# Optimization experiments

Hardware: AMD Instinct MI355X
Metric: run time of the kernel (lower is better)

Reference implementation:

```python
import jax, jax.numpy as jnp
import numpy as np

B, N, E, M, F_, H, K, D, T = 16, 100, 9900, 50, 64, 128, 20, 2, 8
EPS = 1e-5

def _lin(key, fin, fout):
    k1, _ = jax.random.split(key)
    w = jax.random.normal(k1, (fin, fout), jnp.float32) * np.float32(np.sqrt(2.0 / (fin + fout)))
    b = jnp.full((fout,), 0.1, jnp.float32)
    return w, b

def setup_inputs():
    key = jax.random.key(0)
    ks = jax.random.split(key, 16)
    pairs = np.array([(i, j) for i in range(N) for j in range(N) if i != j], np.int64)
    rel_rec = np.zeros((E, N), np.float32); rel_rec[np.arange(E), pairs[:, 0]] = 1.0
    rel_send = np.zeros((E, N), np.float32); rel_send[np.arange(E), pairs[:, 1]] = 1.0
    W1g, b1g = _lin(ks[0], 2 * F_, H)
    W2g, b2g = _lin(ks[1], H, H)
    W1h, b1h = _lin(ks[2], F_, H)
    W2h, b2h = _lin(ks[3], H, H)
    Wo1, bo1 = _lin(ks[4], 2 * H, H)
    Wa, ba = _lin(ks[5], H, K)
    Wm, bm = _lin(ks[6], H, K * D)
    ones = jnp.ones((H,), jnp.float32); zeros = jnp.zeros((H,), jnp.float32)
    return {
        'data': jax.random.normal(ks[7], (B, N, T, D), jnp.float32),
        'rel_rec_g': jnp.asarray(rel_rec), 'rel_send_g': jnp.asarray(rel_send),
        'rel_type_g': jax.random.uniform(ks[8], (B, E, 4), jnp.float32),
        'rel_type_hg': jax.random.uniform(ks[9], (B, M, 4), jnp.float32),
        'I_HG': jax.random.uniform(ks[10], (B, N, M), jnp.float32),
        'v_combined': jax.random.normal(ks[11], (B, N, F_), jnp.float32),
        'W1g': W1g, 'b1g': b1g, 'g1g': ones, 'be1g': zeros,
        'W2g': W2g, 'b2g': b2g, 'g2g': ones, 'be2g': zeros,
        'W1h': W1h, 'b1h': b1h, 'g1h': ones, 'be1h': zeros,
        'W2h': W2h, 'b2h': b2h, 'g2h': ones, 'be2h': zeros,
        'Wo1': Wo1, 'bo1': bo1, 'Wa': Wa, 'ba': ba, 'Wm': Wm, 'bm': bm,
        'output_steps': 8,
    }

def _lrelu(x):
    return jnp.where(x >= 0, x, 0.01 * x)

def _bn(x, g, b):
    # training-mode BatchNorm1d: batch statistics over the flattened row dim
    mu = x.mean(0); var = x.var(0)
    return (x - mu) / jnp.sqrt(var + EPS) * g + b

def reference(data, rel_rec_g, rel_send_g, rel_type_g, rel_type_hg, I_HG, v_combined,
              W1g, b1g, g1g, be1g, W2g, b2g, g2g, be2g,
              W1h, b1h, g1h, be1h, W2h, b2h, g2h, be2h,
              Wo1, bo1, Wa, ba, Wm, bm, output_steps):
    inputs = jnp.swapaxes(data, 1, 2)                                # [B,T,N,D]
    # ---- CG edge branch (step-invariant: depends only on v_combined) ----
    recv = jnp.einsum('en,bnf->bef', rel_rec_g, v_combined)
    send = jnp.einsum('en,bnf->bef', rel_send_g, v_combined)
    pre = jnp.concatenate([recv, send], -1)                          # [B,E,2F]
    x = pre.reshape(B * E, 2 * F_)
    msg = _lrelu(_bn(x @ W1g + b1g, g1g, be1g))
    msg = _lrelu(_bn(msg @ W2g + b2g, g2g, be2g)).reshape(B, E, H)
    # (msg[...,None] * Z).mean(-1) == msg * Z.mean(-1) since Z is independent of the hid dim
    all_g = _lrelu(msg * rel_type_g.mean(-1, keepdims=True) + pre)   # identity shortcut (n_in_mlp == n_hid)
    hidden_g = jnp.einsum('beh,en->bnh', all_g, rel_send_g) / D
    # ---- hypergraph branch ----
    pre_h = jnp.einsum('bnm,bnf->bmf', I_HG, v_combined)             # [B,M,F]
    xh = pre_h.reshape(B * M, F_)
    mh = _lrelu(_bn(xh @ W1h + b1h, g1h, be1h))
    mh = _lrelu(_bn(mh @ W2h + b2h, g2h, be2h)).reshape(B, M, H)
    hidden_hg = jnp.einsum('bmh,bnm->bnh', mh * rel_type_hg.mean(-1, keepdims=True), I_HG) / D
    # ---- output heads ----
    v = _lrelu(jnp.concatenate([hidden_g, hidden_hg], -1) @ Wo1 + bo1)  # [B,N,H]
    alpha = jax.nn.softmax(v @ Wa + ba, -1)                          # [B,N,K]
    mu_base = (v @ Wm + bm).reshape(B, N, K, D)
    core = jnp.einsum('bnk,bnkd->bnd', alpha, mu_base)               # sample_core == mixture mean
    nkey = jax.random.key(1234)
    preds, mus = [], []
    ins = inputs[:, 0]                                               # burn_in_steps = 1
    for s in range(output_steps):
        if s > 0:
            ins = preds[-1]
        noise = jax.random.normal(jax.random.fold_in(nkey, s), (B, N, D), jnp.float32)  # sigma == 1
        preds.append(ins + core + noise)
        mus.append(mu_base + ins[:, :, None, :])                     # in-place mu += inputs in torch
    S = output_steps
    preds_out = jnp.swapaxes(jnp.stack(preds, 1), 1, 2)              # [B,N,S,D]
    alphas = jnp.broadcast_to(alpha[:, :, None, :], (B, N, S, K))
    mus_out = jnp.stack(mus, 2)                                      # [B,N,S,K,D]
    sigmas = jnp.ones((B, N, S, K, D), jnp.float32)
    return (preds_out, alphas, mus_out, sigmas)
```

## Files before the change

kernel.cpp:

```cpp
#include <hip/hip_runtime.h>

#define BB 16
#define NN 100
#define EE 9900
#define MM 50
#define FF 64
#define KK 20
#define DD 2
#define ROWS (BB*EE)
#define HROWS (BB*MM)
#define BN_CNT (BB*NN)
#define NTILE (ROWS/64)
#define GEMMB 512
#define EPSF 1e-5f
#define XPITCH 136

typedef __attribute__((ext_vector_type(8))) short bf16x8;
typedef __attribute__((ext_vector_type(4))) float f32x4;

__device__ __forceinline__ float lrelu(float x) { return (x >= 0.f) ? x : 0.01f * x; }

__device__ __forceinline__ unsigned short f2bf(float x) {
  unsigned u = __float_as_uint(x);
  return (unsigned short)((u + 0x7fffu + ((u >> 16) & 1u)) >> 16);
}
__device__ __forceinline__ unsigned pk2(float a, float b) {
  return (unsigned)f2bf(a) | ((unsigned)f2bf(b) << 16);
}
__device__ __forceinline__ float bf2f(unsigned short u) {
  return __uint_as_float(((unsigned)u) << 16);
}

__device__ __forceinline__ void tf2x32(unsigned k0, unsigned k1,
                                       unsigned x0, unsigned x1,
                                       unsigned& o0, unsigned& o1) {
  unsigned ks2 = k0 ^ k1 ^ 0x1BD11BDAu;
  x0 += k0; x1 += k1;
#define TFR(r) { x0 += x1; x1 = (x1 << r) | (x1 >> (32 - r)); x1 ^= x0; }
  TFR(13) TFR(15) TFR(26) TFR(6)   x0 += k1;  x1 += ks2 + 1u;
  TFR(17) TFR(29) TFR(16) TFR(24)  x0 += ks2; x1 += k0 + 2u;
  TFR(13) TFR(15) TFR(26) TFR(6)   x0 += k0;  x1 += k1 + 3u;
  TFR(17) TFR(29) TFR(16) TFR(24)  x0 += k1;  x1 += ks2 + 4u;
  TFR(13) TFR(15) TFR(26) TFR(6)   x0 += ks2; x1 += k0 + 5u;
#undef TFR
  o0 = x0; o1 = x1;
}

__device__ __forceinline__ float bits_to_normal(unsigned bits) {
  float f = __uint_as_float((bits >> 9) | 0x3f800000u) - 1.0f;
  const float lo = -0.99999994f;
  float x = fmaxf(lo, fmaf(f, 2.0f, lo));
  float w = -log1pf(-x * x);
  float p;
  if (w < 5.0f) {
    w = w - 2.5f;
    p = 2.81022636e-08f;
    p = fmaf(p, w, 3.43273939e-07f);
    p = fmaf(p, w, -3.5233877e-06f);
    p = fmaf(p, w, -4.39150654e-06f);
    p = fmaf(p, w, 0.00021858087f);
    p = fmaf(p, w, -0.00125372503f);
    p = fmaf(p, w, -0.00417768164f);
    p = fmaf(p, w, 0.246640727f);
    p = fmaf(p, w, 1.50140941f);
  } else {
    w = sqrtf(w) - 3.0f;
    p = -0.000200214257f;
    p = fmaf(p, w, 0.000100950558f);
    p = fmaf(p, w, 0.00134934322f);
    p = fmaf(p, w, -0.00367342844f);
    p = fmaf(p, w, 0.00573950773f);
    p = fmaf(p, w, -0.0076224613f);
    p = fmaf(p, w, 0.00943887047f);
    p = fmaf(p, w, 1.00167406f);
    p = fmaf(p, w, 2.83297682f);
  }
  return 1.41421356237f * (p * x);
}

struct SmemGemm {
  unsigned short Xt[64 * XPITCH];
  float aColP[132], bColP[132];
  float bsum[128], bssq[128];
};
struct SmemVe {
  float cat[2][256], vres[2][128], lgs[2][KK], mrow[2][KK * DD], alsh[2][KK];
};
struct SmemH {
  float prerow[2][FF];
  float trow[2][128];
};
struct SmemOut {
  float nz[4][8][2], ins[4][8][2], alsh[4][KK];
};

struct Params {
  const float *data, *rtg, *rth, *I_HG, *v;
  const float *W1g, *b1g, *g1g, *be1g, *W2g, *b2g, *g2g, *be2g;
  const float *W1h, *b1h, *g1h, *be1h, *W2h, *b2h, *g2h, *be2h;
  const float *Wo1, *bo1, *Wa, *ba, *Wm, *bm;
  unsigned short *Ybf, *WtG;
  float *stats1, *stats2, *statsh1, *statsh2, *scaleg, *scaleh;
  float *hg, *hh, *y1h, *y2h, *va, *vmu, *vcore, *partials, *partial2;
  float *out;
};


__device__ __forceinline__ void prep_phase(const Params& p, int bid, int nblk, int tid) {
  for (int i = bid * 256 + tid; i < ROWS + HROWS; i += nblk * 256) {
    if (i < ROWS) {
      float4 r = ((const float4*)p.rtg)[i];
      p.scaleg[i] = (r.x + r.y + r.z + r.w) * 0.25f;
    } else {
      float4 r = ((const float4*)p.rth)[i - ROWS];
      p.scaleh[i - ROWS] = (r.x + r.y + r.z + r.w) * 0.25f;
    }
  }
  for (int i = bid * 256 + tid; i < 32768; i += nblk * 256) {
    int w = i >> 14, rem = i & 16383;
    int c = rem & 127, k = rem >> 7;
    const float* W = w ? p.W2g : p.W1g;
    p.WtG[w * 16384 + c * 128 + k] = f2bf(W[k * 128 + c]);
  }
}

template <int MODE>
__device__ __forceinline__ void edge_gemm_phase(
    const Params& p, SmemGemm& sg, int bid, int nblk, int tid,
    const unsigned short* WtG, const unsigned short* Yin, unsigned short* Yout,
    const float* bias, const float* gmm, const float* beta,
    const float* stats_in) {
  const int lane = tid & 63, wid = tid >> 6;
  const int l15 = lane & 15, lq = lane >> 4;
  const int cb = wid * 32;
  const int rsi = tid >> 2, q = tid & 3, k0 = q * 32;

  if (tid < 128) {
    sg.bsum[tid] = 0.f; sg.bssq[tid] = 0.f;
    if (MODE == 1) {
      float s = stats_in[tid], ss = stats_in[128 + tid];
      float mu = s * (1.f / ROWS);
      float var = fmaxf(ss * (1.f / ROWS) - mu * mu, 0.f);
      float rs = 1.f / sqrtf(var + EPSF);
      float a = rs * gmm[tid];
      int pi = tid + (tid >> 5);
      sg.aColP[pi] = a; sg.bColP[pi] = beta[tid] - mu * a;
    }
  }

  const unsigned short* WA = WtG + (cb + l15) * 128 + lq * 8;
  bf16x8 a0[4], a1[4];
#pragma unroll
  for (int kc = 0; kc < 4; ++kc) {
    a0[kc] = *(const bf16x8*)(WA + kc * 32);
    a1[kc] = *(const bf16x8*)(WA + 16 * 128 + kc * 32);
  }
  float4 bi0 = *(const float4*)&bias[cb + lq * 4];
  float4 bi1 = *(const float4*)&bias[cb + 16 + lq * 4];
  f32x4 bv0 = {bi0.x, bi0.y, bi0.z, bi0.w};
  f32x4 bv1 = {bi1.x, bi1.y, bi1.z, bi1.w};
  f32x4 s0 = {0.f,0.f,0.f,0.f}, ss0 = {0.f,0.f,0.f,0.f};
  f32x4 s1 = {0.f,0.f,0.f,0.f}, ss1 = {0.f,0.f,0.f,0.f};

  float4 ra[4], rb[4];
  uint4  rw[4];

  auto LOAD = [&](int tile) {
    if (MODE == 0) {
      int g = tile * 64 + rsi;
      int b = g / EE; int e = g - b * EE;
      int i = e / 99; int jj = e - i * 99; int j = jj + ((jj >= i) ? 1 : 0);
      int vsrc = (q < 2) ? ((b * NN + i) * FF + q * 32)
                         : ((b * NN + j) * FF + (q - 2) * 32);
#pragma unroll
      for (int i2 = 0; i2 < 4; ++i2) {
        ra[i2] = *(const float4*)&p.v[vsrc + i2 * 8];
        rb[i2] = *(const float4*)&p.v[vsrc + i2 * 8 + 4];
      }
    } else {
      const unsigned short* src = Yin + (size_t)(tile * 64 + rsi) * 128 + k0;
#pragma unroll
      for (int i2 = 0; i2 < 4; ++i2) rw[i2] = *(const uint4*)&src[i2 * 8];
    }
  };
  auto WRITE = [&]() {
    if (MODE == 0) {
#pragma unroll
      for (int i2 = 0; i2 < 4; ++i2) {
        uint4 pk;
        pk.x = pk2(ra[i2].x, ra[i2].y); pk.y = pk2(ra[i2].z, ra[i2].w);
        pk.z = pk2(rb[i2].x, rb[i2].y); pk.w = pk2(rb[i2].z, rb[i2].w);
        *(uint4*)&sg.Xt[rsi * XPITCH + k0 + i2 * 8] = pk;
      }
    } else {
#pragma unroll
      for (int i2 = 0; i2 < 4; ++i2) {
        unsigned rr[4] = {rw[i2].x, rw[i2].y, rw[i2].z, rw[i2].w};
        unsigned ow[4];
#pragma unroll
        for (int u = 0; u < 4; ++u) {
          int k = k0 + i2 * 8 + u * 2;
          int p1 = k + (k >> 5);
          float xl = __uint_as_float(rr[u] << 16);
          float xh = __uint_as_float(rr[u] & 0xffff0000u);
          xl = lrelu(fmaf(xl, sg.aColP[p1], sg.bColP[p1]));
          xh = lrelu(fmaf(xh, sg.aColP[p1 + 1], sg.bColP[p1 + 1]));
          ow[u] = pk2(xl, xh);
        }
        uint4 pk; pk.x = ow[0]; pk.y = ow[1]; pk.z = ow[2]; pk.w = ow[3];
        *(uint4*)&sg.Xt[rsi * XPITCH + k0 + i2 * 8] = pk;
      }
    }
  };

  if (MODE == 1) __syncthreads();

  LOAD(bid);
  for (int t = bid; t < NTILE; t += nblk) {
    if (t != bid) __syncthreads();
    WRITE();
    if (t + nblk < NTILE) LOAD(t + nblk);
    __syncthreads();

    f32x4 acc[2][4];
#pragma unroll
    for (int a = 0; a < 2; ++a)
#pragma unroll
      for (int b2 = 0; b2 < 4; ++b2) acc[a][b2] = (f32x4){0.f, 0.f, 0.f, 0.f};
    const unsigned short* Bb = &sg.Xt[l15 * XPITCH + lq * 8];
#pragma unroll
    for (int kc = 0; kc < 4; ++kc) {
      int ko = kc * 32;
#pragma unroll
      for (int rbi = 0; rbi < 4; ++rbi) {
        bf16x8 bfr = *(const bf16x8*)(Bb + rbi * 16 * XPITCH + ko);
        acc[0][rbi] = __builtin_amdgcn_mfma_f32_16x16x32_bf16(a0[kc], bfr, acc[0][rbi], 0, 0, 0);
        acc[1][rbi] = __builtin_amdgcn_mfma_f32_16x16x32_bf16(a1[kc], bfr, acc[1][rbi], 0, 0, 0);
      }
    }

    int r0 = t * 64;
#pragma unroll
    for (int rbi = 0; rbi < 4; ++rbi) {
      size_t r = (size_t)(r0 + rbi * 16 + l15);
      f32x4 y0 = acc[0][rbi] + bv0;
      f32x4 y1 = acc[1][rbi] + bv1;
      uint2 w0; w0.x = pk2(y0.x, y0.y); w0.y = pk2(y0.z, y0.w);
      uint2 w1; w1.x = pk2(y1.x, y1.y); w1.y = pk2(y1.z, y1.w);
      *(uint2*)&Yout[r * 128 + cb + lq * 4] = w0;
      *(uint2*)&Yout[r * 128 + cb + 16 + lq * 4] = w1;
      s0 += y0; ss0 += y0 * y0;
      s1 += y1; ss1 += y1 * y1;
    }
  }

#pragma unroll
  for (int u = 0; u < 4; ++u) {
    atomicAdd(&sg.bsum[cb + lq * 4 + u], s0[u]);
    atomicAdd(&sg.bssq[cb + lq * 4 + u], ss0[u]);
    atomicAdd(&sg.bsum[cb + 16 + lq * 4 + u], s1[u]);
    atomicAdd(&sg.bssq[cb + 16 + lq * 4 + u], ss1[u]);
  }
  __syncthreads();
  if (tid < 128) {
    p.partials[(size_t)bid * 256 + tid] = sg.bsum[tid];
    p.partials[(size_t)bid * 256 + 128 + tid] = sg.bssq[tid];
  }
}

__device__ __forceinline__ void redA_phase(const float* partials, float* partial2,
                                           int nblk, int bid, int tid) {
  if (bid < 32) {
    float s = 0.f;
    for (int r = bid; r < nblk; r += 32) s += partials[(size_t)r * 256 + tid];
    partial2[bid * 256 + tid] = s;
  }
}
__device__ __forceinline__ void redB_phase(const float* partial2, float* stats,
                                           int bid, int tid) {
  if (bid == 0) {
    float s = 0.f;
#pragma unroll
    for (int r = 0; r < 32; ++r) s += partial2[r * 256 + tid];
    stats[tid] = s;
  }
}

__device__ __forceinline__ void recv_phase(const Params& p, int bid, int nblk, int tid) {
  const int sub = tid >> 7, h = tid & 127;
  float s = p.stats2[h], ss = p.stats2[128 + h];
  float mu = s * (1.f / ROWS);
  float var = fmaxf(ss * (1.f / ROWS) - mu * mu, 0.f);
  float rs = 1.f / sqrtf(var + EPSF);
  float a = rs * p.g2g[h]; float bc = p.be2g[h] - mu * a;
  for (int bn = bid * 2 + sub; bn < BN_CNT; bn += 2 * nblk) {
    int b = bn / NN, n = bn - b * NN;
    float sv = (h >= 64) ? p.v[(b * NN + n) * FF + (h - 64)] : 0.f;
    float acc = 0.f;
#pragma unroll 4
    for (int i = 0; i < NN; ++i) {
      if (i == n) continue;
      int e = i * 99 + ((n < i) ? n : n - 1);
      int row = b * EE + e;
      float y = bf2f(p.Ybf[(size_t)row * 128 + h]);
      float msgv = lrelu(y * a + bc);
      float pre = (h < 64) ? p.v[(b * NN + i) * FF + h] : sv;
      float ag = lrelu(fmaf(msgv, p.scaleg[row], pre));
      acc += ag;
    }
    p.hg[bn * 128 + h] = acc * 0.5f;
  }
}

__device__ __forceinline__ void h1_phase(const Params& p, SmemH& sh, int bid, int nblk, int tid) {
  const int sub = tid >> 7, ht = tid & 127;
  for (int bm = bid * 2 + sub; bm < HROWS; bm += 2 * nblk) {
    int b = bm / MM, m = bm - b * MM;
    if (ht < FF) {
      float s = 0.f;
      for (int n = 0; n < NN; ++n)
        s = fmaf(p.I_HG[(b * NN + n) * MM + m], p.v[(b * NN + n) * FF + ht], s);
      sh.prerow[sub][ht] = s;
    }
    __syncthreads();
    float y = p.b1h[ht];
    for (int f = 0; f < FF; ++f) y = fmaf(sh.prerow[sub][f], p.W1h[f * 128 + ht], y);
    p.y1h[bm * 128 + ht] = y;
    __syncthreads();
  }
}

__device__ __forceinline__ void cs_phase(const float* X, float* stats, int bid, int tid) {
  if (bid < 32) {
    int c = bid * 4 + (tid >> 6), rt = tid & 63;
    float s = 0.f, ss = 0.f;
    for (int r = rt; r < HROWS; r += 64) {
      float x = X[(size_t)r * 128 + c];
      s += x; ss += x * x;
    }
    for (int off = 32; off; off >>= 1) {
      s += __shfl_down(s, off, 64);
      ss += __shfl_down(ss, off, 64);
    }
    if (rt == 0) { stats[c] = s; stats[128 + c] = ss; }
  }
}

__device__ __forceinline__ void h2_phase(const Params& p, SmemH& sh, int bid, int nblk, int tid) {
  const int sub = tid >> 7, ht = tid & 127;
  float s = p.statsh1[ht], ss = p.statsh1[128 + ht];
  float mu = s * (1.f / HROWS);
  float var = fmaxf(ss * (1.f / HROWS) - mu * mu, 0.f);
  float rs = 1.f / sqrtf(var + EPSF);
  float a = rs * p.g1h[ht]; float bc = p.be1h[ht] - mu * a;
  for (int bm = bid * 2 + sub; bm < HROWS; bm += 2 * nblk) {
    sh.trow[sub][ht] = lrelu(p.y1h[bm * 128 + ht] * a + bc);
    __syncthreads();
    float y = p.b2h[ht];
    for (int f = 0; f < 128; ++f) y = fmaf(sh.trow[sub][f], p.W2h[f * 128 + ht], y);
    p.y2h[bm * 128 + ht] = y;
    __syncthreads();
  }
}

__device__ __forceinline__ void h3_phase(const Params& p, int bid, int nblk, int tid) {
  const int sub = tid >> 7, h = tid & 127;
  float s = p.statsh2[h], ss = p.statsh2[128 + h];
  float mu = s * (1.f / HROWS);
  float var = fmaxf(ss * (1.f / HROWS) - mu * mu, 0.f);
  float rs = 1.f / sqrtf(var + EPSF);
  float a = rs * p.g2h[h]; float bc = p.be2h[h] - mu * a;
  for (int bn = bid * 2 + sub; bn < BN_CNT; bn += 2 * nblk) {
    int b = bn / NN, n = bn - b * NN;
    float acc = 0.f;
    for (int m = 0; m < MM; ++m) {
      float x = lrelu(p.y2h[(b * MM + m) * 128 + h] * a + bc);
      acc = fmaf(x * p.scaleh[b * MM + m], p.I_HG[(b * NN + n) * MM + m], acc);
    }
    p.hh[bn * 128 + h] = acc * 0.5f;
  }
}

__device__ __forceinline__ void ve_phase(const Params& p, SmemVe& sv, int bid, int nblk, int tid) {
  const int sub = tid >> 7, ht = tid & 127;
  for (int bn = bid * 2 + sub; bn < BN_CNT; bn += 2 * nblk) {
    sv.cat[sub][ht] = p.hg[bn * 128 + ht];
    sv.cat[sub][128 + ht] = p.hh[bn * 128 + ht];
    __syncthreads();
    float vv = p.bo1[ht];
    for (int k = 0; k < 256; ++k)
      vv = fmaf(sv.cat[sub][k], p.Wo1[k * 128 + ht], vv);
    sv.vres[sub][ht] = lrelu(vv);
    __syncthreads();
    if (ht < KK) {
      float s = p.ba[ht];
      for (int f = 0; f < 128; ++f) s = fmaf(sv.vres[sub][f], p.Wa[f * KK + ht], s);
      sv.lgs[sub][ht] = s;
    } else if (ht >= 64 && ht < 64 + KK * DD) {
      int c = ht - 64;
      float s = p.bm[c];
      for (int f = 0; f < 128; ++f) s = fmaf(sv.vres[sub][f], p.Wm[f * (KK * DD) + c], s);
      sv.mrow[sub][c] = s;
      p.vmu[bn * (KK * DD) + c] = s;
    }
    __syncthreads();
    if (ht < KK) {
      float mx = sv.lgs[sub][0];
      for (int k2 = 1; k2 < KK; ++k2) mx = fmaxf(mx, sv.lgs[sub][k2]);
      float se = 0.f;
      for (int k2 = 0; k2 < KK; ++k2) se += expf(sv.lgs[sub][k2] - mx);
      float al = expf(sv.lgs[sub][ht] - mx) / se;
      sv.alsh[sub][ht] = al;
      p.va[bn * KK + ht] = al;
    }
    __syncthreads();
    if (ht < DD) {
      float s = 0.f;
      for (int k2 = 0; k2 < KK; ++k2)
        s = fmaf(sv.alsh[sub][k2], sv.mrow[sub][k2 * DD + ht], s);
      p.vcore[bn * DD + ht] = s;
    }
    __syncthreads();
  }
}

__device__ __forceinline__ void out_phase(const Params& p, SmemOut& so, int bid, int nblk, int tid) {
  const int ut = tid >> 6, t = tid & 63;
  for (int bn = bid * 4 + ut; bn < BN_CNT; bn += 4 * nblk) {
    if (t < 16) {
      int s = t >> 1, d = t & 1;
      unsigned fk0, fk1;
      tf2x32(0u, 1234u, 0u, (unsigned)s, fk0, fk1);
      unsigned flat = (unsigned)(bn * 2 + d);
      unsigned o0, o1;
      tf2x32(fk0, fk1, 0u, flat, o0, o1);
      so.nz[ut][s][d] = bits_to_normal(o0 ^ o1);
    }
    if (t < KK) so.alsh[ut][t] = p.va[bn * KK + t];
    __syncthreads();
    if (t < 2) {
      int d = t;
      float ins0 = p.data[bn * 16 + d];
      float core = p.vcore[bn * 2 + d];
      float pp = ins0;
      for (int s = 0; s < 8; ++s) {
        so.ins[ut][s][d] = pp;
        pp = (pp + core) + so.nz[ut][s][d];
        p.out[(bn * 8 + s) * 2 + d] = pp;
      }
    }
    __syncthreads();
    for (int q = t; q < 160; q += 64) {
      int k = q % KK;
      p.out[25600 + bn * 160 + q] = so.alsh[ut][k];
    }
    for (int q = t; q < 320; q += 64) {
      int s = q / 40, kd = q - s * 40, d = kd & 1;
      p.out[281600 + bn * 320 + q] = p.vmu[bn * 40 + kd] + so.ins[ut][s][d];
    }
    for (int q = t; q < 320; q += 64) p.out[793600 + bn * 320 + q] = 1.0f;
    __syncthreads();
  }
}

__global__ __launch_bounds__(256) void k_prepW(Params p) {
  prep_phase(p, blockIdx.x, gridDim.x, threadIdx.x);
}
__global__ __launch_bounds__(256, 2) void k_gemm0W(Params p) {
  __shared__ __align__(16) SmemGemm sg;
  edge_gemm_phase<0>(p, sg, blockIdx.x, gridDim.x, threadIdx.x, p.WtG, nullptr,
                     p.Ybf, p.b1g, nullptr, nullptr, nullptr);
}
__global__ __launch_bounds__(256, 2) void k_gemm1W(Params p) {
  __shared__ __align__(16) SmemGemm sg;
  edge_gemm_phase<1>(p, sg, blockIdx.x, gridDim.x, threadIdx.x, p.WtG + 16384,
                     p.Ybf, p.Ybf, p.b2g, p.g1g, p.be1g, p.stats1);
}
__global__ __launch_bounds__(256) void k_redAW(const float* partials, float* partial2, int nblk) {
  redA_phase(partials, partial2, nblk, blockIdx.x, threadIdx.x);
}
__global__ __launch_bounds__(256) void k_redBW(const float* partial2, float* stats) {
  redB_phase(partial2, stats, blockIdx.x, threadIdx.x);
}
__global__ __launch_bounds__(256) void k_recvW(Params p) {
  recv_phase(p, blockIdx.x, gridDim.x, threadIdx.x);
}
__global__ __launch_bounds__(256) void k_h1W(Params p) {
  __shared__ SmemH sh;
  h1_phase(p, sh, blockIdx.x, gridDim.x, threadIdx.x);
}
__global__ __launch_bounds__(256) void k_csW(const float* X, float* stats) {
  cs_phase(X, stats, blockIdx.x, threadIdx.x);
}
__global__ __launch_bounds__(256) void k_h2W(Params p) {
  __shared__ SmemH sh;
  h2_phase(p, sh, blockIdx.x, gridDim.x, threadIdx.x);
}
__global__ __launch_bounds__(256) void k_h3W(Params p) {
  h3_phase(p, blockIdx.x, gridDim.x, threadIdx.x);
}
__global__ __launch_bounds__(256) void k_veW(Params p) {
  __shared__ SmemVe sv;
  ve_phase(p, sv, blockIdx.x, gridDim.x, threadIdx.x);
}
__global__ __launch_bounds__(256) void k_outW(Params p) {
  __shared__ SmemOut so;
  out_phase(p, so, blockIdx.x, gridDim.x, threadIdx.x);
}

extern "C" void kernel_launch(void* const* d_in, const int* in_sizes, int n_in,
                              void* d_out, int out_size, void* d_ws, size_t ws_size,
                              hipStream_t stream) {
  char* wsb = (char*)d_ws;

  Params p;
  p.data = (const float*)d_in[0];
  p.rtg  = (const float*)d_in[3];
  p.rth  = (const float*)d_in[4];
  p.I_HG = (const float*)d_in[5];
  p.v    = (const float*)d_in[6];
  p.W1g  = (const float*)d_in[7];
  p.b1g  = (const float*)d_in[8];
  p.g1g  = (const float*)d_in[9];
  p.be1g = (const float*)d_in[10];
  p.W2g  = (const float*)d_in[11];
  p.b2g  = (const float*)d_in[12];
  p.g2g  = (const float*)d_in[13];
  p.be2g = (const float*)d_in[14];
  p.W1h  = (const float*)d_in[15];
  p.b1h  = (const float*)d_in[16];
  p.g1h  = (const float*)d_in[17];
  p.be1h = (const float*)d_in[18];
  p.W2h  = (const float*)d_in[19];
  p.b2h  = (const float*)d_in[20];
  p.g2h  = (const float*)d_in[21];
  p.be2h = (const float*)d_in[22];
  p.Wo1  = (const float*)d_in[23];
  p.bo1  = (const float*)d_in[24];
  p.Wa   = (const float*)d_in[25];
  p.ba   = (const float*)d_in[26];
  p.Wm   = (const float*)d_in[27];
  p.bm   = (const float*)d_in[28];

  p.Ybf     = (unsigned short*)wsb;
  p.stats1  = (float*)(wsb + 40550400);
  p.stats2  = p.stats1 + 256;
  p.statsh1 = p.stats2 + 256;
  p.statsh2 = p.statsh1 + 256;
  p.scaleg  = (float*)(wsb + 40550400 + 4096);
  p.scaleh  = p.scaleg + ROWS;
  p.hg      = p.scaleh + HROWS;
  p.hh      = p.hg + BN_CNT * 128;
  p.y1h     = p.hh + BN_CNT * 128;
  p.y2h     = p.y1h + HROWS * 128;
  p.va      = p.y2h + HROWS * 128;
  p.vmu     = p.va + BN_CNT * KK;
  p.vcore   = p.vmu + BN_CNT * KK * DD;
  p.WtG     = (unsigned short*)(p.vcore + BN_CNT * DD);
  p.partials = (float*)(p.WtG + 2 * 16384);
  p.partial2 = p.partials + (size_t)GEMMB * 256;
  p.out     = (float*)d_out;

  k_prepW<<<256, 256, 0, stream>>>(p);
  k_gemm0W<<<GEMMB, 256, 0, stream>>>(p);
  k_redAW<<<32, 256, 0, stream>>>(p.partials, p.partial2, GEMMB);
  k_redBW<<<1, 256, 0, stream>>>(p.partial2, p.stats1);
  k_gemm1W<<<GEMMB, 256, 0, stream>>>(p);
  k_redAW<<<32, 256, 0, stream>>>(p.partials, p.partial2, GEMMB);
  k_redBW<<<1, 256, 0, stream>>>(p.partial2, p.stats2);
  k_recvW<<<800, 256, 0, stream>>>(p);
  k_h1W<<<400, 256, 0, stream>>>(p);
  k_csW<<<32, 256, 0, stream>>>(p.y1h, p.statsh1);
  k_h2W<<<400, 256, 0, stream>>>(p);
  k_csW<<<32, 256, 0, stream>>>(p.y2h, p.statsh2);
  k_h3W<<<800, 256, 0, stream>>>(p);
  k_veW<<<800, 256, 0, stream>>>(p);
  k_outW<<<400, 256, 0, stream>>>(p);
}
```

Measured before the change: 303.3 us.

## Fuse reductions into last-block epilogues and merge tail phases into one kernel

Batch-statistic reductions now run in the last block to finish each GEMM or hypergraph kernel, using an atomic counter, which removes the separate redA/redB/cs launches. The receive, hypergraph-aggregate, output-head and output-write phases are merged into a single per-node kernel, so the hg/hh/va/vmu/vcore intermediates no longer go through global memory. GEMM grid grows to 825 blocks with launch bounds raised to 4 waves per SIMD. This cuts the launch count from 15 to 6. In exchange, the final reduction is serialized in one block, and the counters depend on being reset in the prep kernel each call.

Result: slower. 624.7 us (+106.0%).

```diff
diff --git a/kernel.cpp b/kernel.cpp
--- a/kernel.cpp
+++ b/kernel.cpp
@@ -11,7 +11,7 @@
 #define HROWS (BB*MM)
 #define BN_CNT (BB*NN)
 #define NTILE (ROWS/64)
-#define GEMMB 512
+#define GEMMB 825
 #define EPSF 1e-5f
 #define XPITCH 136
 
@@ -83,16 +83,6 @@
   float aColP[132], bColP[132];
   float bsum[128], bssq[128];
 };
-struct SmemVe {
-  float cat[2][256], vres[2][128], lgs[2][KK], mrow[2][KK * DD], alsh[2][KK];
-};
-struct SmemH {
-  float prerow[2][FF];
-  float trow[2][128];
-};
-struct SmemOut {
-  float nz[4][8][2], ins[4][8][2], alsh[4][KK];
-};
 
 struct Params {
   const float *data, *rtg, *rth, *I_HG, *v;
@@ -101,13 +91,15 @@
   const float *Wo1, *bo1, *Wa, *ba, *Wm, *bm;
   unsigned short *Ybf, *WtG;
   float *stats1, *stats2, *statsh1, *statsh2, *scaleg, *scaleh;
-  float *hg, *hh, *y1h, *y2h, *va, *vmu, *vcore, *partials, *partial2;
+  float *y1h, *y2h, *partials;
+  unsigned *cnt;
   float *out;
 };
 
-
-__device__ __forceinline__ void prep_phase(const Params& p, int bid, int nblk, int tid) {
-  for (int i = bid * 256 + tid; i < ROWS + HROWS; i += nblk * 256) {
+__global__ __launch_bounds__(256) void k_prepW(Params p) {
+  const int bid = blockIdx.x, tid = threadIdx.x;
+  if (bid == 0 && tid < 4) p.cnt[tid] = 0;
+  for (int i = bid * 256 + tid; i < ROWS + HROWS; i += 256 * 256) {
     if (i < ROWS) {
       float4 r = ((const float4*)p.rtg)[i];
       p.scaleg[i] = (r.x + r.y + r.z + r.w) * 0.25f;
@@ -116,11 +108,14 @@
       p.scaleh[i - ROWS] = (r.x + r.y + r.z + r.w) * 0.25f;
     }
   }
-  for (int i = bid * 256 + tid; i < 32768; i += nblk * 256) {
-    int w = i >> 14, rem = i & 16383;
-    int c = rem & 127, k = rem >> 7;
-    const float* W = w ? p.W2g : p.W1g;
-    p.WtG[w * 16384 + c * 128 + k] = f2bf(W[k * 128 + c]);
+  {
+    int i = bid * 256 + tid;
+    if (i < 32768) {
+      int w = i >> 14, rem = i & 16383;
+      int c = rem & 127, k = rem >> 7;
+      const float* W = w ? p.W2g : p.W1g;
+      p.WtG[w * 16384 + c * 128 + k] = f2bf(W[k * 128 + c]);
+    }
   }
 }
 
@@ -268,244 +263,203 @@
   }
 }
 
-__device__ __forceinline__ void redA_phase(const float* partials, float* partial2,
-                                           int nblk, int bid, int tid) {
-  if (bid < 32) {
+__device__ __forceinline__ void lastblock_stats(const Params& p, float* stats,
+                                                unsigned* cnt, int nblk, int tid) {
+  __shared__ int isLast;
+  __threadfence();
+  __syncthreads();
+  if (tid == 0) isLast = (atomicAdd(cnt, 1u) == (unsigned)(nblk - 1));
+  __syncthreads();
+  if (isLast) {
+    __threadfence();
     float s = 0.f;
-    for (int r = bid; r < nblk; r += 32) s += partials[(size_t)r * 256 + tid];
-    partial2[bid * 256 + tid] = s;
-  }
-}
-__device__ __forceinline__ void redB_phase(const float* partial2, float* stats,
-                                           int bid, int tid) {
-  if (bid == 0) {
+#pragma unroll 5
+    for (int r = 0; r < nblk; ++r) s += p.partials[(size_t)r * 256 + tid];
+    stats[tid] = s;
+  }
+}
+
+__global__ __launch_bounds__(256, 4) void k_gemm0W(Params p) {
+  __shared__ __align__(16) SmemGemm sg;
+  edge_gemm_phase<0>(p, sg, blockIdx.x, GEMMB, threadIdx.x, p.WtG, nullptr,
+                     p.Ybf, p.b1g, nullptr, nullptr, nullptr);
+  lastblock_stats(p, p.stats1, p.cnt + 0, GEMMB, threadIdx.x);
+}
+__global__ __launch_bounds__(256, 4) void k_gemm1W(Params p) {
+  __shared__ __align__(16) SmemGemm sg;
+  edge_gemm_phase<1>(p, sg, blockIdx.x, GEMMB, threadIdx.x, p.WtG + 16384,
+                     p.Ybf, p.Ybf, p.b2g, p.g1g, p.be1g, p.stats1);
+  lastblock_stats(p, p.stats2, p.cnt + 1, GEMMB, threadIdx.x);
+}
+
+__device__ __forceinline__ void lastblock_colstats(const float* X, float* stats,
+                                                   unsigned* cnt, int nblk, int tid) {
+  __shared__ int isLast;
+  __shared__ float rs[128], rss[128];
+  __threadfence();
+  __syncthreads();
+  if (tid == 0) isLast = (atomicAdd(cnt, 1u) == (unsigned)(nblk - 1));
+  __syncthreads();
+  if (isLast) {
+    __threadfence();
+    int c = tid & 127, half = tid >> 7;
+    float s = 0.f, ss = 0.f;
+    for (int r = half * 400; r < half * 400 + 400; ++r) {
+      float x = X[(size_t)r * 128 + c];
+      s += x; ss += x * x;
+    }
+    if (half) { rs[c] = s; rss[c] = ss; }
+    __syncthreads();
+    if (!half) { stats[c] = s + rs[c]; stats[128 + c] = ss + rss[c]; }
+  }
+}
+
+__global__ __launch_bounds__(256) void k_h1W(Params p) {
+  __shared__ float prerow[2][FF];
+  const int bid = blockIdx.x, tid = threadIdx.x;
+  const int sub = tid >> 7, ht = tid & 127;
+  const int bm = bid * 2 + sub;
+  const int b = bm / MM, m = bm - b * MM;
+  if (ht < FF) {
     float s = 0.f;
-#pragma unroll
-    for (int r = 0; r < 32; ++r) s += partial2[r * 256 + tid];
-    stats[tid] = s;
-  }
-}
-
-__device__ __forceinline__ void recv_phase(const Params& p, int bid, int nblk, int tid) {
-  const int sub = tid >> 7, h = tid & 127;
-  float s = p.stats2[h], ss = p.stats2[128 + h];
-  float mu = s * (1.f / ROWS);
-  float var = fmaxf(ss * (1.f / ROWS) - mu * mu, 0.f);
+    for (int n = 0; n < NN; ++n)
+      s = fmaf(p.I_HG[(b * NN + n) * MM + m], p.v[(b * NN + n) * FF + ht], s);
+    prerow[sub][ht] = s;
+  }
+  __syncthreads();
+  float y = p.b1h[ht];
+  for (int f = 0; f < FF; ++f) y = fmaf(prerow[sub][f], p.W1h[f * 128 + ht], y);
+  p.y1h[bm * 128 + ht] = y;
+  lastblock_colstats(p.y1h, p.statsh1, p.cnt + 2, 400, tid);
+}
+
+__global__ __launch_bounds__(256) void k_h2W(Params p) {
+  __shared__ float trow[2][128];
+  const int bid = blockIdx.x, tid = threadIdx.x;
+  const int sub = tid >> 7, ht = tid & 127;
+  const int bm = bid * 2 + sub;
+  float s = p.statsh1[ht], ss = p.statsh1[128 + ht];
+  float mu = s * (1.f / HROWS);
+  float var = fmaxf(ss * (1.f / HROWS) - mu * mu, 0.f);
   float rs = 1.f / sqrtf(var + EPSF);
-  float a = rs * p.g2g[h]; float bc = p.be2g[h] - mu * a;
-  for (int bn = bid * 2 + sub; bn < BN_CNT; bn += 2 * nblk) {
-    int b = bn / NN, n = bn - b * NN;
-    float sv = (h >= 64) ? p.v[(b * NN + n) * FF + (h - 64)] : 0.f;
+  float a = rs * p.g1h[ht]; float bc = p.be1h[ht] - mu * a;
+  trow[sub][ht] = lrelu(p.y1h[bm * 128 + ht] * a + bc);
+  __syncthreads();
+  float y = p.b2h[ht];
+  for (int f = 0; f < 128; ++f) y = fmaf(trow[sub][f], p.W2h[f * 128 + ht], y);
+  p.y2h[bm * 128 + ht] = y;
+  lastblock_colstats(p.y2h, p.statsh2, p.cnt + 3, 400, tid);
+}
+
+struct SmemFin {
+  float cat[2][256];
+  float vres[2][128];
+  float lgs[2][KK], mrow[2][KK * DD], alsh[2][KK], vcore[2][DD];
+  float nz[2][8][2], ins[2][8][2];
+};
+
+__global__ __launch_bounds__(256) void k_finW(Params p) {
+  __shared__ __align__(16) SmemFin sm;
+  const int tid = threadIdx.x;
+  const int sub = tid >> 7, ht = tid & 127;
+  const int bn = blockIdx.x * 2 + sub;
+  const int b = bn / NN, n = bn - b * NN;
+
+  if (ht < 16) {
+    int s = ht >> 1, d = ht & 1;
+    unsigned fk0, fk1;
+    tf2x32(0u, 1234u, 0u, (unsigned)s, fk0, fk1);
+    unsigned flat = (unsigned)(bn * 2 + d);
+    unsigned o0, o1;
+    tf2x32(fk0, fk1, 0u, flat, o0, o1);
+    sm.nz[sub][s][d] = bits_to_normal(o0 ^ o1);
+  }
+
+  {
+    float s = p.stats2[ht], ss = p.stats2[128 + ht];
+    float mu = s * (1.f / ROWS);
+    float var = fmaxf(ss * (1.f / ROWS) - mu * mu, 0.f);
+    float rs = 1.f / sqrtf(var + EPSF);
+    float a = rs * p.g2g[ht]; float bc = p.be2g[ht] - mu * a;
+    float sv = (ht >= 64) ? p.v[(b * NN + n) * FF + (ht - 64)] : 0.f;
     float acc = 0.f;
 #pragma unroll 4
     for (int i = 0; i < NN; ++i) {
       if (i == n) continue;
       int e = i * 99 + ((n < i) ? n : n - 1);
       int row = b * EE + e;
-      float y = bf2f(p.Ybf[(size_t)row * 128 + h]);
+      float y = bf2f(p.Ybf[(size_t)row * 128 + ht]);
       float msgv = lrelu(y * a + bc);
-      float pre = (h < 64) ? p.v[(b * NN + i) * FF + h] : sv;
-      float ag = lrelu(fmaf(msgv, p.scaleg[row], pre));
-      acc += ag;
-    }
-    p.hg[bn * 128 + h] = acc * 0.5f;
-  }
-}
-
-__device__ __forceinline__ void h1_phase(const Params& p, SmemH& sh, int bid, int nblk, int tid) {
-  const int sub = tid >> 7, ht = tid & 127;
-  for (int bm = bid * 2 + sub; bm < HROWS; bm += 2 * nblk) {
-    int b = bm / MM, m = bm - b * MM;
-    if (ht < FF) {
-      float s = 0.f;
-      for (int n = 0; n < NN; ++n)
-        s = fmaf(p.I_HG[(b * NN + n) * MM + m], p.v[(b * NN + n) * FF + ht], s);
-      sh.prerow[sub][ht] = s;
-    }
-    __syncthreads();
-    float y = p.b1h[ht];
-    for (int f = 0; f < FF; ++f) y = fmaf(sh.prerow[sub][f], p.W1h[f * 128 + ht], y);
-    p.y1h[bm * 128 + ht] = y;
-    __syncthreads();
-  }
-}
-
-__device__ __forceinline__ void cs_phase(const float* X, float* stats, int bid, int tid) {
-  if (bid < 32) {
-    int c = bid * 4 + (tid >> 6), rt = tid & 63;
-    float s = 0.f, ss = 0.f;
-    for (int r = rt; r < HROWS; r += 64) {
-      float x = X[(size_t)r * 128 + c];
-      s += x; ss += x * x;
-    }
-    for (int off = 32; off; off >>= 1) {
-      s += __shfl_down(s, off, 64);
-      ss += __shfl_down(ss, off, 64);
-    }
-    if (rt == 0) { stats[c] = s; stats[128 + c] = ss; }
-  }
-}
-
-__device__ __forceinline__ void h2_phase(const Params& p, SmemH& sh, int bid, int nblk, int tid) {
-  const int sub = tid >> 7, ht = tid & 127;
-  float s = p.statsh1[ht], ss = p.statsh1[128 + ht];
-  float mu = s * (1.f / HROWS);
-  float var = fmaxf(ss * (1.f / HROWS) - mu * mu, 0.f);
-  float rs = 1.f / sqrtf(var + EPSF);
-  float a = rs * p.g1h[ht]; float bc = p.be1h[ht] - mu * a;
-  for (int bm = bid * 2 + sub; bm < HROWS; bm += 2 * nblk) {
-    sh.trow[sub][ht] = lrelu(p.y1h[bm * 128 + ht] * a + bc);
-    __syncthreads();
-    float y = p.b2h[ht];
-    for (int f = 0; f < 128; ++f) y = fmaf(sh.trow[sub][f], p.W2h[f * 128 + ht], y);
-    p.y2h[bm * 128 + ht] = y;
-    __syncthreads();
-  }
-}
-
-__device__ __forceinline__ void h3_phase(const Params& p, int bid, int nblk, int tid) {
-  const int sub = tid >> 7, h = tid & 127;
-  float s = p.statsh2[h], ss = p.statsh2[128 + h];
-  float mu = s * (1.f / HROWS);
-  float var = fmaxf(ss * (1.f / HROWS) - mu * mu, 0.f);
-  float rs = 1.f / sqrtf(var + EPSF);
-  float a = rs * p.g2h[h]; float bc = p.be2h[h] - mu * a;
-  for (int bn = bid * 2 + sub; bn < BN_CNT; bn += 2 * nblk) {
-    int b = bn / NN, n = bn - b * NN;
+      float pre = (ht < 64) ? p.v[(b * NN + i) * FF + ht] : sv;
+      acc += lrelu(fmaf(msgv, p.scaleg[row], pre));
+    }
+    sm.cat[sub][ht] = acc * 0.5f;
+  }
+  {
+    float s = p.statsh2[ht], ss = p.statsh2[128 + ht];
+    float mu = s * (1.f / HROWS);
+    float var = fmaxf(ss * (1.f / HROWS) - mu * mu, 0.f);
+    float rs = 1.f / sqrtf(var + EPSF);
+    float a = rs * p.g2h[ht]; float bc = p.be2h[ht] - mu * a;
     float acc = 0.f;
     for (int m = 0; m < MM; ++m) {
-      float x = lrelu(p.y2h[(b * MM + m) * 128 + h] * a + bc);
+      float x = lrelu(p.y2h[(b * MM + m) * 128 + ht] * a + bc);
       acc = fmaf(x * p.scaleh[b * MM + m], p.I_HG[(b * NN + n) * MM + m], acc);
     }
-    p.hh[bn * 128 + h] = acc * 0.5f;
-  }
-}
-
-__device__ __forceinline__ void ve_phase(const Params& p, SmemVe& sv, int bid, int nblk, int tid) {
-  const int sub = tid >> 7, ht = tid & 127;
-  for (int bn = bid * 2 + sub; bn < BN_CNT; bn += 2 * nblk) {
-    sv.cat[sub][ht] = p.hg[bn * 128 + ht];
-    sv.cat[sub][128 + ht] = p.hh[bn * 128 + ht];
-    __syncthreads();
-    float vv = p.bo1[ht];
-    for (int k = 0; k < 256; ++k)
-      vv = fmaf(sv.cat[sub][k], p.Wo1[k * 128 + ht], vv);
-    sv.vres[sub][ht] = lrelu(vv);
-    __syncthreads();
-    if (ht < KK) {
-      float s = p.ba[ht];
-      for (int f = 0; f < 128; ++f) s = fmaf(sv.vres[sub][f], p.Wa[f * KK + ht], s);
-      sv.lgs[sub][ht] = s;
-    } else if (ht >= 64 && ht < 64 + KK * DD) {
-      int c = ht - 64;
-      float s = p.bm[c];
-      for (int f = 0; f < 128; ++f) s = fmaf(sv.vres[sub][f], p.Wm[f * (KK * DD) + c], s);
-      sv.mrow[sub][c] = s;
-      p.vmu[bn * (KK * DD) + c] = s;
-    }
-    __syncthreads();
-    if (ht < KK) {
-      float mx = sv.lgs[sub][0];
-      for (int k2 = 1; k2 < KK; ++k2) mx = fmaxf(mx, sv.lgs[sub][k2]);
-      float se = 0.f;
-      for (int k2 = 0; k2 < KK; ++k2) se += expf(sv.lgs[sub][k2] - mx);
-      float al = expf(sv.lgs[sub][ht] - mx) / se;
-      sv.alsh[sub][ht] = al;
-      p.va[bn * KK + ht] = al;
-    }
-    __syncthreads();
-    if (ht < DD) {
-      float s = 0.f;
-      for (int k2 = 0; k2 < KK; ++k2)
-        s = fmaf(sv.alsh[sub][k2], sv.mrow[sub][k2 * DD + ht], s);
-      p.vcore[bn * DD + ht] = s;
-    }
-    __syncthreads();
-  }
-}
-
-__device__ __forceinline__ void out_phase(const Params& p, SmemOut& so, int bid, int nblk, int tid) {
-  const int ut = tid >> 6, t = tid & 63;
-  for (int bn = bid * 4 + ut; bn < BN_CNT; bn += 4 * nblk) {
-    if (t < 16) {
-      int s = t >> 1, d = t & 1;
-      unsigned fk0, fk1;
-      tf2x32(0u, 1234u, 0u, (unsigned)s, fk0, fk1);
-      unsigned flat = (unsigned)(bn * 2 + d);
-      unsigned o0, o1;
-      tf2x32(fk0, fk1, 0u, flat, o0, o1);
-      so.nz[ut][s][d] = bits_to_normal(o0 ^ o1);
-    }
-    if (t < KK) so.alsh[ut][t] = p.va[bn * KK + t];
-    __syncthreads();
-    if (t < 2) {
-      int d = t;
-      float ins0 = p.data[bn * 16 + d];
-      float core = p.vcore[bn * 2 + d];
-      float pp = ins0;
-      for (int s = 0; s < 8; ++s) {
-        so.ins[ut][s][d] = pp;
-        pp = (pp + core) + so.nz[ut][s][d];
-        p.out[(bn * 8 + s) * 2 + d] = pp;
-      }
-    }
-    __syncthreads();
-    for (int q = t; q < 160; q += 64) {
-      int k = q % KK;
-      p.out[25600 + bn * 160 + q] = so.alsh[ut][k];
-    }
-    for (int q = t; q < 320; q += 64) {
-      int s = q / 40, kd = q - s * 40, d = kd & 1;
-      p.out[281600 + bn * 320 + q] = p.vmu[bn * 40 + kd] + so.ins[ut][s][d];
-    }
-    for (int q = t; q < 320; q += 64) p.out[793600 + bn * 320 + q] = 1.0f;
-    __syncthreads();
-  }
-}
-
-__global__ __launch_bounds__(256) void k_prepW(Params p) {
-  prep_phase(p, blockIdx.x, gridDim.x, threadIdx.x);
-}
-__global__ __launch_bounds__(256, 2) void k_gemm0W(Params p) {
-  __shared__ __align__(16) SmemGemm sg;
-  edge_gemm_phase<0>(p, sg, blockIdx.x, gridDim.x, threadIdx.x, p.WtG, nullptr,
-                     p.Ybf, p.b1g, nullptr, nullptr, nullptr);
-}
-__global__ __launch_bounds__(256, 2) void k_gemm1W(Params p) {
-  __shared__ __align__(16) SmemGemm sg;
-  edge_gemm_phase<1>(p, sg, blockIdx.x, gridDim.x, threadIdx.x, p.WtG + 16384,
-                     p.Ybf, p.Ybf, p.b2g, p.g1g, p.be1g, p.stats1);
-}
-__global__ __launch_bounds__(256) void k_redAW(const float* partials, float* partial2, int nblk) {
-  redA_phase(partials, partial2, nblk, blockIdx.x, threadIdx.x);
-}
-__global__ __launch_bounds__(256) void k_redBW(const float* partial2, float* stats) {
-  redB_phase(partial2, stats, blockIdx.x, threadIdx.x);
-}
-__global__ __launch_bounds__(256) void k_recvW(Params p) {
-  recv_phase(p, blockIdx.x, gridDim.x, threadIdx.x);
-}
-__global__ __launch_bounds__(256) void k_h1W(Params p) {
-  __shared__ SmemH sh;
-  h1_phase(p, sh, blockIdx.x, gridDim.x, threadIdx.x);
-}
-__global__ __launch_bounds__(256) void k_csW(const float* X, float* stats) {
-  cs_phase(X, stats, blockIdx.x, threadIdx.x);
-}
-__global__ __launch_bounds__(256) void k_h2W(Params p) {
-  __shared__ SmemH sh;
-  h2_phase(p, sh, blockIdx.x, gridDim.x, threadIdx.x);
-}
-__global__ __launch_bounds__(256) void k_h3W(Params p) {
-  h3_phase(p, blockIdx.x, gridDim.x, threadIdx.x);
-}
-__global__ __launch_bounds__(256) void k_veW(Params p) {
-  __shared__ SmemVe sv;
-  ve_phase(p, sv, blockIdx.x, gridDim.x, threadIdx.x);
-}
-__global__ __launch_bounds__(256) void k_outW(Params p) {
-  __shared__ SmemOut so;
-  out_phase(p, so, blockIdx.x, gridDim.x, threadIdx.x);
+    sm.cat[sub][128 + ht] = acc * 0.5f;
+  }
+  __syncthreads();
+
+  float vv = p.bo1[ht];
+  for (int k = 0; k < 256; ++k)
+    vv = fmaf(sm.cat[sub][k], p.Wo1[k * 128 + ht], vv);
+  sm.vres[sub][ht] = lrelu(vv);
+  __syncthreads();
+  if (ht < KK) {
+    float s = p.ba[ht];
+    for (int f = 0; f < 128; ++f) s = fmaf(sm.vres[sub][f], p.Wa[f * KK + ht], s);
+    sm.lgs[sub][ht] = s;
+  } else if (ht >= 64 && ht < 64 + KK * DD) {
+    int c = ht - 64;
+    float s = p.bm[c];
+    for (int f = 0; f < 128; ++f) s = fmaf(sm.vres[sub][f], p.Wm[f * (KK * DD) + c], s);
+    sm.mrow[sub][c] = s;
+  }
+  __syncthreads();
+  if (ht < KK) {
+    float mx = sm.lgs[sub][0];
+    for (int k2 = 1; k2 < KK; ++k2) mx = fmaxf(mx, sm.lgs[sub][k2]);
+    float se = 0.f;
+    for (int k2 = 0; k2 < KK; ++k2) se += expf(sm.lgs[sub][k2] - mx);
+    sm.alsh[sub][ht] = expf(sm.lgs[sub][ht] - mx) / se;
+  }
+  __syncthreads();
+  if (ht < DD) {
+    float s = 0.f;
+    for (int k2 = 0; k2 < KK; ++k2)
+      s = fmaf(sm.alsh[sub][k2], sm.mrow[sub][k2 * DD + ht], s);
+    sm.vcore[sub][ht] = s;
+  }
+  __syncthreads();
+
+  if (ht < 2) {
+    int d = ht;
+    float pp = p.data[bn * 16 + d];
+    float core = sm.vcore[sub][d];
+    for (int s = 0; s < 8; ++s) {
+      sm.ins[sub][s][d] = pp;
+      pp = (pp + core) + sm.nz[sub][s][d];
+      p.out[(bn * 8 + s) * 2 + d] = pp;
+    }
+  }
+  __syncthreads();
+  for (int q = ht; q < 160; q += 128)
+    p.out[25600 + bn * 160 + q] = sm.alsh[sub][q % KK];
+  for (int q = ht; q < 320; q += 128) {
+    int s = q / 40, kd = q - s * 40, d = kd & 1;
+    p.out[281600 + bn * 320 + q] = sm.mrow[sub][kd] + sm.ins[sub][s][d];
+  }
+  for (int q = ht; q < 320; q += 128) p.out[793600 + bn * 320 + q] = 1.0f;
 }
 
 extern "C" void kernel_launch(void* const* d_in, const int* in_sizes, int n_in,
@@ -549,31 +503,17 @@
   p.statsh2 = p.statsh1 + 256;
   p.scaleg  = (float*)(wsb + 40550400 + 4096);
   p.scaleh  = p.scaleg + ROWS;
-  p.hg      = p.scaleh + HROWS;
-  p.hh      = p.hg + BN_CNT * 128;
-  p.y1h     = p.hh + BN_CNT * 128;
+  p.y1h     = p.scaleh + HROWS;
   p.y2h     = p.y1h + HROWS * 128;
-  p.va      = p.y2h + HROWS * 128;
-  p.vmu     = p.va + BN_CNT * KK;
-  p.vcore   = p.vmu + BN_CNT * KK * DD;
-  p.WtG     = (unsigned short*)(p.vcore + BN_CNT * DD);
+  p.WtG     = (unsigned short*)(p.y2h + HROWS * 128);
   p.partials = (float*)(p.WtG + 2 * 16384);
-  p.partial2 = p.partials + (size_t)GEMMB * 256;
+  p.cnt     = (unsigned*)(p.partials + (size_t)GEMMB * 256);
   p.out     = (float*)d_out;
 
   k_prepW<<<256, 256, 0, stream>>>(p);
   k_gemm0W<<<GEMMB, 256, 0, stream>>>(p);
-  k_redAW<<<32, 256, 0, stream>>>(p.partials, p.partial2, GEMMB);
-  k_redBW<<<1, 256, 0, stream>>>(p.partial2, p.stats1);
   k_gemm1W<<<GEMMB, 256, 0, stream>>>(p);
-  k_redAW<<<32, 256, 0, stream>>>(p.partials, p.partial2, GEMMB);
-  k_redBW<<<1, 256, 0, stream>>>(p.partial2, p.stats2);
-  k_recvW<<<800, 256, 0, stream>>>(p);
   k_h1W<<<400, 256, 0, stream>>>(p);
-  k_csW<<<32, 256, 0, stream>>>(p.y1h, p.statsh1);
   k_h2W<<<400, 256, 0, stream>>>(p);
-  k_csW<<<32, 256, 0, stream>>>(p.y2h, p.statsh2);
-  k_h3W<<<800, 256, 0, stream>>>(p);
-  k_veW<<<800, 256, 0, stream>>>(p);
-  k_outW<<<400, 256, 0, stream>>>(p);
-}
+  k_finW<<<800, 256, 0, stream>>>(p);
+}
```
